# Performance work log

Measured on AMD Instinct MI355X. Metric: run time of the kernel, lower is better.

## Reference

```python
import jax, jax.numpy as jnp
import numpy as np

NX, NY = 512, 1024  # scaled grid (source used 128x256)
HID = 32


def _grid_edges(nx, ny):
    """Bidirectional 4-neighbor grid adjacency as [2, E] int32."""
    idx = np.arange(nx * ny).reshape(nx, ny)
    h_s, h_t = idx[:, :-1].ravel(), idx[:, 1:].ravel()
    v_s, v_t = idx[:-1, :].ravel(), idx[1:, :].ravel()
    src = np.concatenate([h_s, h_t, v_s, v_t])
    dst = np.concatenate([h_t, h_s, v_t, v_s])
    return jnp.asarray(np.stack([src, dst]), dtype=jnp.int32)


def setup_inputs() -> dict:
    key = jax.random.key(0)
    ks = jax.random.split(key, 8)

    def lin(k, fan_in, fan_out):
        bound = 1.0 / np.sqrt(fan_in)
        kw, kb = jax.random.split(k)
        w = jax.random.uniform(kw, (fan_in, fan_out), jnp.float32, -bound, bound)
        b = jax.random.uniform(kb, (fan_out,), jnp.float32, -bound, bound)
        return w, b

    inp = {}
    inp["x"] = jax.random.normal(ks[0], (NX * NY, 4), jnp.float32)
    inp["edge_index_0"] = _grid_edges(NX, NY)
    inp["edge_index_1"] = _grid_edges(NX // 2, NY // 2)
    inp["edge_index_2"] = _grid_edges(NX // 4, NY // 4)
    inp["fc1_w"], inp["fc1_b"] = lin(ks[1], 4, HID)
    for i in range(1, 6):
        inp[f"w{i}"], inp[f"b{i}"] = lin(ks[1 + i], HID, HID)
    inp["fc2_w"], inp["fc2_b"] = lin(ks[7], HID, 2)
    return inp


def gcn_conv(x, edge_index, w, b):
    """PyG GCNConv: self-loops + symmetric norm + linear + scatter-add + bias."""
    n = x.shape[0]
    loop = jnp.arange(n, dtype=edge_index.dtype)
    src = jnp.concatenate([edge_index[0], loop])
    dst = jnp.concatenate([edge_index[1], loop])
    deg = jax.ops.segment_sum(jnp.ones(dst.shape, x.dtype), dst, num_segments=n)
    dis = jax.lax.rsqrt(deg)  # deg >= 1 because of self-loops
    norm = dis[src] * dis[dst]  # [E+N]
    xw = x @ w  # [N, HID]
    out = jax.ops.segment_sum(xw[src] * norm[:, None], dst, num_segments=n)
    return out + b


def _upsample2(x):
    # Buffer-exact replica of torch `upsample(x, dim=2, channels=32, scale=2)`:
    # with `channels` doubling between iterations; then transpose + reshape.
    x = x.T  # [32, N]
    ch = HID
    for _ in range(2):
        x = jnp.repeat(x.reshape(ch, -1), 2, axis=-1)
        ch *= 2
    return x.T.reshape(-1, HID)  # [4N, 32]


def reference(x, edge_index_0, edge_index_1, edge_index_2,
              fc1_w, fc1_b, w1, b1, w2, b2, w3, b3, w4, b4, w5, b5,
              fc2_w, fc2_b):
    nx1, ny1 = NX // 2, NY // 2
    h = jax.nn.relu(x @ fc1_w + fc1_b)
    h = jax.nn.relu(gcn_conv(h, edge_index_0, w1, b1))            # level 0
    h1 = h.reshape(NX, NY, HID)[::2, ::2, :].reshape(-1, HID)     # down to level 1
    h1 = jax.nn.relu(gcn_conv(h1, edge_index_1, w2, b2))
    h2 = h1.reshape(nx1, ny1, HID)[::2, ::2, :].reshape(-1, HID)  # down to level 2
    h2 = jax.nn.relu(gcn_conv(h2, edge_index_2, w3, b3))
    h1u = h1 + _upsample2(h2)                                     # up to level 1
    h1u = jax.nn.relu(gcn_conv(h1u, edge_index_1, w4, b4))
    hu = h + _upsample2(h1u)                                      # up to level 0
    hu = jax.nn.relu(gcn_conv(hu, edge_index_0, w5, b5))
    return hu @ fc2_w + fc2_b  # [NX*NY, 2]
```

## Files before the change

### kernel.cpp

```cpp
#include <hip/hip_runtime.h>


#define TI 8
#define TJ 32

__device__ __forceinline__ float disf(int i, int j, int nx, int ny) {
  int deg = 1 + (i > 0) + (i < nx - 1) + (j > 0) + (j < ny - 1);
  return rsqrtf((float)deg);
}

__device__ __forceinline__ float4 f4z() { return make_float4(0.f, 0.f, 0.f, 0.f); }
__device__ __forceinline__ float4 f4fma(float s, float4 w, float4 a) {
  a.x = fmaf(s, w.x, a.x); a.y = fmaf(s, w.y, a.y);
  a.z = fmaf(s, w.z, a.z); a.w = fmaf(s, w.w, a.w);
  return a;
}
__device__ __forceinline__ float4 f4add(float4 a, float4 b) {
  return make_float4(a.x + b.x, a.y + b.y, a.z + b.z, a.w + b.w);
}
__device__ __forceinline__ float4 f4scale(float4 a, float s) {
  return make_float4(a.x * s, a.y * s, a.z * s, a.w * s);
}

template <int MODE, int NX, int NY, int NLOW>
__device__ __forceinline__ float4 load_u(
    const float* __restrict__ src, const float* __restrict__ low,
    const float4 (&f1c)[4], const float4& f1b, int gi, int gj, int c) {
  if (gi < 0 || gi >= NX || gj < 0 || gj >= NY) return f4z();
  const float d = disf(gi, gj, NX, NY);
  if constexpr (MODE == 0) {
    const float4 xv = ((const float4*)src)[gi * NY + gj];
    float4 h;
    h.x = fmaxf(fmaf(xv.x, f1c[0].x, fmaf(xv.y, f1c[1].x, fmaf(xv.z, f1c[2].x, fmaf(xv.w, f1c[3].x, f1b.x)))), 0.f);
    h.y = fmaxf(fmaf(xv.x, f1c[0].y, fmaf(xv.y, f1c[1].y, fmaf(xv.z, f1c[2].y, fmaf(xv.w, f1c[3].y, f1b.y)))), 0.f);
    h.z = fmaxf(fmaf(xv.x, f1c[0].z, fmaf(xv.y, f1c[1].z, fmaf(xv.z, f1c[2].z, fmaf(xv.w, f1c[3].z, f1b.z)))), 0.f);
    h.w = fmaxf(fmaf(xv.x, f1c[0].w, fmaf(xv.y, f1c[1].w, fmaf(xv.z, f1c[2].w, fmaf(xv.w, f1c[3].w, f1b.w)))), 0.f);
    return f4scale(h, d);
  } else if constexpr (MODE == 1) {
    const float4 v = ((const float4*)src)[((size_t)(2 * gi) * (2 * NY) + 2 * gj) * 8 + c];
    return f4scale(v, d);
  } else {
    const int r = gi * NY + gj;
    float4 v = ((const float4*)src)[(size_t)r * 8 + c];
    const int col = 16 * (r & 1) + 2 * c;
    const float2 E = *(const float2*)(low + (size_t)(r >> 3) * 32 + col);
    const float2 O = *(const float2*)(low + (size_t)((NLOW + (r >> 2)) >> 1) * 32 + col);
    v.x += E.x; v.y += O.x; v.z += E.y; v.w += O.y;
    return f4scale(v, d);
  }
}

template <int MODE, int NX, int NY, int NLOW>
__global__ __launch_bounds__(256, 4) void fused_gcn(
    const float* __restrict__ src, const float* __restrict__ low,
    const float* __restrict__ w, const float* __restrict__ bias,
    const float* __restrict__ fc1w, const float* __restrict__ fc1b,
    const float* __restrict__ fw2, const float* __restrict__ fb2,
    float* __restrict__ out) {
  __shared__ float sT[32][TI * TJ + 4];
  __shared__ float ldsW[1024];
  __shared__ float ldsB[104];

  const int t = threadIdx.x;
  ((float4*)ldsW)[t] = ((const float4*)w)[t];
  if (t < 32) ldsB[t] = bias[t];
  if constexpr (MODE == 3) {
    if (t >= 32 && t < 96) ldsB[t] = fw2[t - 32];
    if (t >= 96 && t < 98) ldsB[t] = fb2[t - 96];
  }

  const int jn = t >> 3, c = t & 7;
  const int j0 = blockIdx.x * TJ, i0 = blockIdx.y * TI;
  const int gj = j0 + jn;

  float4 f1c[4], f1b;
  if constexpr (MODE == 0) {
#pragma unroll
    for (int r = 0; r < 4; ++r) f1c[r] = *(const float4*)(fc1w + r * 32 + 4 * c);
    f1b = *(const float4*)(fc1b + 4 * c);
  }
  auto LOADU = [&](int a, int b) -> float4 {
    return load_u<MODE, NX, NY, NLOW>(src, low, f1c, f1b, a, b, c);
  };

  float4 up = LOADU(i0 - 1, gj);
  float4 uc = LOADU(i0, gj);
  float4 un = LOADU(i0 + 1, gj);
  float4 lf = LOADU(i0, gj - 1);
  float4 rt = LOADU(i0, gj + 1);

#pragma unroll
  for (int i = 0; i < TI; ++i) {
    const float4 sv = f4add(f4add(f4add(up, uc), f4add(un, lf)), rt);
    const int n = i * TJ + jn;
    sT[4 * c + 0][n] = sv.x; sT[4 * c + 1][n] = sv.y;
    sT[4 * c + 2][n] = sv.z; sT[4 * c + 3][n] = sv.w;
    if (i < TI - 1) {
      up = uc; uc = un;
      un = LOADU(i0 + i + 2, gj);
      lf = LOADU(i0 + i + 1, gj - 1);
      rt = LOADU(i0 + i + 1, gj + 1);
    }
  }
  __syncthreads();

  const int tn = t >> 2, tc = t & 3;
  float4 o00 = f4z(), o01 = f4z(), o10 = f4z(), o11 = f4z();
  float4 o20 = f4z(), o21 = f4z(), o30 = f4z(), o31 = f4z();
#pragma unroll
  for (int k = 0; k < 32; ++k) {
    const float4 sv = *(const float4*)&sT[k][4 * tn];
    const float4 w0 = *(const float4*)&ldsW[k * 32 + 8 * tc];
    const float4 w1 = *(const float4*)&ldsW[k * 32 + 8 * tc + 4];
    o00 = f4fma(sv.x, w0, o00); o01 = f4fma(sv.x, w1, o01);
    o10 = f4fma(sv.y, w0, o10); o11 = f4fma(sv.y, w1, o11);
    o20 = f4fma(sv.z, w0, o20); o21 = f4fma(sv.z, w1, o21);
    o30 = f4fma(sv.w, w0, o30); o31 = f4fma(sv.w, w1, o31);
  }
  const float4 b0 = *(const float4*)&ldsB[8 * tc];
  const float4 b1 = *(const float4*)&ldsB[8 * tc + 4];

  float4 fwA = f4z(), fwB = f4z(), fwC = f4z(), fwD = f4z();
  if constexpr (MODE == 3) {
    fwA = *(const float4*)&ldsB[32 + 16 * tc];
    fwB = *(const float4*)&ldsB[32 + 16 * tc + 4];
    fwC = *(const float4*)&ldsB[32 + 16 * tc + 8];
    fwD = *(const float4*)&ldsB[32 + 16 * tc + 12];
  }

  float4 oo[4][2] = {{o00, o01}, {o10, o11}, {o20, o21}, {o30, o31}};
  float a0[4], a1[4];
#pragma unroll
  for (int nn = 0; nn < 4; ++nn) {
    const int n = 4 * tn + nn;
    const int gi = i0 + (n >> 5), gjo = j0 + (n & 31);
    const float dv = disf(gi, gjo, NX, NY);
    float4 v0, v1;
    v0.x = fmaxf(fmaf(dv, oo[nn][0].x, b0.x), 0.f);
    v0.y = fmaxf(fmaf(dv, oo[nn][0].y, b0.y), 0.f);
    v0.z = fmaxf(fmaf(dv, oo[nn][0].z, b0.z), 0.f);
    v0.w = fmaxf(fmaf(dv, oo[nn][0].w, b0.w), 0.f);
    v1.x = fmaxf(fmaf(dv, oo[nn][1].x, b1.x), 0.f);
    v1.y = fmaxf(fmaf(dv, oo[nn][1].y, b1.y), 0.f);
    v1.z = fmaxf(fmaf(dv, oo[nn][1].z, b1.z), 0.f);
    v1.w = fmaxf(fmaf(dv, oo[nn][1].w, b1.w), 0.f);
    if constexpr (MODE != 3) {
      float* op = out + (size_t)(gi * NY + gjo) * 32 + 8 * tc;
      *(float4*)op = v0;
      *(float4*)(op + 4) = v1;
    } else {
      a0[nn] = v0.x * fwA.x + v0.y * fwA.z + v0.z * fwB.x + v0.w * fwB.z +
               v1.x * fwC.x + v1.y * fwC.z + v1.z * fwD.x + v1.w * fwD.z;
      a1[nn] = v0.x * fwA.y + v0.y * fwA.w + v0.z * fwB.y + v0.w * fwB.w +
               v1.x * fwC.y + v1.y * fwC.w + v1.z * fwD.y + v1.w * fwD.w;
    }
  }
  if constexpr (MODE == 3) {
#pragma unroll
    for (int nn = 0; nn < 4; ++nn) {
      a0[nn] += __shfl_xor(a0[nn], 1, 64); a0[nn] += __shfl_xor(a0[nn], 2, 64);
      a1[nn] += __shfl_xor(a1[nn], 1, 64); a1[nn] += __shfl_xor(a1[nn], 2, 64);
    }
    if (tc == 0) {
      const float fb0 = ldsB[96], fb1 = ldsB[97];
#pragma unroll
      for (int nn = 0; nn < 4; ++nn) {
        const int n = 4 * tn + nn;
        const int gi = i0 + (n >> 5), gjo = j0 + (n & 31);
        ((float2*)out)[gi * NY + gjo] = make_float2(a0[nn] + fb0, a1[nn] + fb1);
      }
    }
  }
}

#define N0 (512 * 1024)
#define N1 (256 * 512)
#define N2 (128 * 256)

extern "C" void kernel_launch(void* const* d_in, const int* in_sizes, int n_in,
                              void* d_out, int out_size, void* d_ws, size_t ws_size,
                              hipStream_t stream) {
  const float* x    = (const float*)d_in[0];
  const float* fc1w = (const float*)d_in[4];
  const float* fc1b = (const float*)d_in[5];
  const float* w1 = (const float*)d_in[6];
  const float* b1 = (const float*)d_in[7];
  const float* w2 = (const float*)d_in[8];
  const float* b2 = (const float*)d_in[9];
  const float* w3 = (const float*)d_in[10];
  const float* b3 = (const float*)d_in[11];
  const float* w4 = (const float*)d_in[12];
  const float* b4 = (const float*)d_in[13];
  const float* w5 = (const float*)d_in[14];
  const float* b5 = (const float*)d_in[15];
  const float* fw2 = (const float*)d_in[16];
  const float* fb2 = (const float*)d_in[17];

  float* ws = (float*)d_ws;
  const size_t S0 = (size_t)N0 * 32, S1 = (size_t)N1 * 32, S2 = (size_t)N2 * 32;
  float* h   = ws;
  float* h1  = ws + S0;
  float* h2  = ws + S0 + S1;
  float* h1u = ws + S0 + S1 + S2;
  float* outp = (float*)d_out;

  fused_gcn<0, 512, 1024, 0><<<dim3(1024 / TJ, 512 / TI), 256, 0, stream>>>(
      x, nullptr, w1, b1, fc1w, fc1b, nullptr, nullptr, h);
  fused_gcn<1, 256, 512, 0><<<dim3(512 / TJ, 256 / TI), 256, 0, stream>>>(
      h, nullptr, w2, b2, nullptr, nullptr, nullptr, nullptr, h1);
  fused_gcn<1, 128, 256, 0><<<dim3(256 / TJ, 128 / TI), 256, 0, stream>>>(
      h1, nullptr, w3, b3, nullptr, nullptr, nullptr, nullptr, h2);
  fused_gcn<2, 256, 512, N2><<<dim3(512 / TJ, 256 / TI), 256, 0, stream>>>(
      h1, h2, w4, b4, nullptr, nullptr, nullptr, nullptr, h1u);
  fused_gcn<3, 512, 1024, N1><<<dim3(1024 / TJ, 512 / TI), 256, 0, stream>>>(
      h, h1u, w5, b5, nullptr, nullptr, fw2, fb2, outp);
}
```

Measured before the change: 218.8 us.

## Halve row tile, remap block IDs for XCD locality, two nodes per thread

Shrinks the tile to 4 rows so each thread computes two nodes instead of four in the 32x32 transform, cutting accumulator registers, and raises the launch-bounds occupancy hint to 6 blocks. Block IDs are swizzled so consecutive tiles are spread in strided groups of eight, aiming to keep spatial neighbours on the same XCD/L2 for halo reuse. LDS padding changes to one float and the final output stores are packed into wider vectors. Smaller tiles add proportionally more halo reloads and per-block weight staging.

```diff
diff --git a/kernel.cpp b/kernel.cpp
--- a/kernel.cpp
+++ b/kernel.cpp
@@ -1,7 +1,7 @@
 #include <hip/hip_runtime.h>
 
 
-#define TI 8
+#define TI 4
 #define TJ 32
 
 __device__ __forceinline__ float disf(int i, int j, int nx, int ny) {
@@ -51,13 +51,13 @@
 }
 
 template <int MODE, int NX, int NY, int NLOW>
-__global__ __launch_bounds__(256, 4) void fused_gcn(
+__global__ __launch_bounds__(256, 6) void fused_gcn(
     const float* __restrict__ src, const float* __restrict__ low,
     const float* __restrict__ w, const float* __restrict__ bias,
     const float* __restrict__ fc1w, const float* __restrict__ fc1b,
     const float* __restrict__ fw2, const float* __restrict__ fb2,
     float* __restrict__ out) {
-  __shared__ float sT[32][TI * TJ + 4];
+  __shared__ float sT[32][TI * TJ + 1];
   __shared__ float ldsW[1024];
   __shared__ float ldsB[104];
 
@@ -69,8 +69,16 @@
     if (t >= 96 && t < 98) ldsB[t] = fb2[t - 96];
   }
 
+  constexpr int GX = NY / TJ;
+  constexpr int GY = NX / TI;
+  constexpr int NWG = GX * GY;
+  constexpr int LGX = (GX == 8) ? 3 : ((GX == 16) ? 4 : 5);
+  const int bid = blockIdx.y * GX + blockIdx.x;
+  const int sw = (bid & 7) * (NWG >> 3) + (bid >> 3);
+  const int j0 = (sw & (GX - 1)) * TJ;
+  const int i0 = (sw >> LGX) * TI;
+
   const int jn = t >> 3, c = t & 7;
-  const int j0 = blockIdx.x * TJ, i0 = blockIdx.y * TI;
   const int gj = j0 + jn;
 
   float4 f1c[4], f1b;
@@ -104,71 +112,63 @@
   }
   __syncthreads();
 
-  const int tn = t >> 2, tc = t & 3;
-  float4 o00 = f4z(), o01 = f4z(), o10 = f4z(), o11 = f4z();
-  float4 o20 = f4z(), o21 = f4z(), o30 = f4z(), o31 = f4z();
+  const int p = t >> 2, tc = t & 3;
+  float4 oA0 = f4z(), oA1 = f4z(), oB0 = f4z(), oB1 = f4z();
 #pragma unroll
   for (int k = 0; k < 32; ++k) {
-    const float4 sv = *(const float4*)&sT[k][4 * tn];
+    const float sa = sT[k][2 * p];
+    const float sb = sT[k][2 * p + 1];
     const float4 w0 = *(const float4*)&ldsW[k * 32 + 8 * tc];
     const float4 w1 = *(const float4*)&ldsW[k * 32 + 8 * tc + 4];
-    o00 = f4fma(sv.x, w0, o00); o01 = f4fma(sv.x, w1, o01);
-    o10 = f4fma(sv.y, w0, o10); o11 = f4fma(sv.y, w1, o11);
-    o20 = f4fma(sv.z, w0, o20); o21 = f4fma(sv.z, w1, o21);
-    o30 = f4fma(sv.w, w0, o30); o31 = f4fma(sv.w, w1, o31);
+    oA0 = f4fma(sa, w0, oA0); oA1 = f4fma(sa, w1, oA1);
+    oB0 = f4fma(sb, w0, oB0); oB1 = f4fma(sb, w1, oB1);
   }
   const float4 b0 = *(const float4*)&ldsB[8 * tc];
   const float4 b1 = *(const float4*)&ldsB[8 * tc + 4];
 
-  float4 fwA = f4z(), fwB = f4z(), fwC = f4z(), fwD = f4z();
-  if constexpr (MODE == 3) {
-    fwA = *(const float4*)&ldsB[32 + 16 * tc];
-    fwB = *(const float4*)&ldsB[32 + 16 * tc + 4];
-    fwC = *(const float4*)&ldsB[32 + 16 * tc + 8];
-    fwD = *(const float4*)&ldsB[32 + 16 * tc + 12];
-  }
-
-  float4 oo[4][2] = {{o00, o01}, {o10, o11}, {o20, o21}, {o30, o31}};
-  float a0[4], a1[4];
-#pragma unroll
-  for (int nn = 0; nn < 4; ++nn) {
-    const int n = 4 * tn + nn;
-    const int gi = i0 + (n >> 5), gjo = j0 + (n & 31);
-    const float dv = disf(gi, gjo, NX, NY);
-    float4 v0, v1;
-    v0.x = fmaxf(fmaf(dv, oo[nn][0].x, b0.x), 0.f);
-    v0.y = fmaxf(fmaf(dv, oo[nn][0].y, b0.y), 0.f);
-    v0.z = fmaxf(fmaf(dv, oo[nn][0].z, b0.z), 0.f);
-    v0.w = fmaxf(fmaf(dv, oo[nn][0].w, b0.w), 0.f);
-    v1.x = fmaxf(fmaf(dv, oo[nn][1].x, b1.x), 0.f);
-    v1.y = fmaxf(fmaf(dv, oo[nn][1].y, b1.y), 0.f);
-    v1.z = fmaxf(fmaf(dv, oo[nn][1].z, b1.z), 0.f);
-    v1.w = fmaxf(fmaf(dv, oo[nn][1].w, b1.w), 0.f);
-    if constexpr (MODE != 3) {
-      float* op = out + (size_t)(gi * NY + gjo) * 32 + 8 * tc;
-      *(float4*)op = v0;
-      *(float4*)(op + 4) = v1;
-    } else {
-      a0[nn] = v0.x * fwA.x + v0.y * fwA.z + v0.z * fwB.x + v0.w * fwB.z +
-               v1.x * fwC.x + v1.y * fwC.z + v1.z * fwD.x + v1.w * fwD.z;
-      a1[nn] = v0.x * fwA.y + v0.y * fwA.w + v0.z * fwB.y + v0.w * fwB.w +
-               v1.x * fwC.y + v1.y * fwC.w + v1.z * fwD.y + v1.w * fwD.w;
-    }
-  }
-  if constexpr (MODE == 3) {
-#pragma unroll
-    for (int nn = 0; nn < 4; ++nn) {
-      a0[nn] += __shfl_xor(a0[nn], 1, 64); a0[nn] += __shfl_xor(a0[nn], 2, 64);
-      a1[nn] += __shfl_xor(a1[nn], 1, 64); a1[nn] += __shfl_xor(a1[nn], 2, 64);
-    }
+  const int nA = 2 * p;
+  const int gi = i0 + (nA >> 5);
+  const int gjA = j0 + (nA & 31);
+  const float dA = disf(gi, gjA, NX, NY);
+  const float dB = disf(gi, gjA + 1, NX, NY);
+
+  float4 vA0, vA1, vB0, vB1;
+  vA0.x = fmaxf(fmaf(dA, oA0.x, b0.x), 0.f); vA0.y = fmaxf(fmaf(dA, oA0.y, b0.y), 0.f);
+  vA0.z = fmaxf(fmaf(dA, oA0.z, b0.z), 0.f); vA0.w = fmaxf(fmaf(dA, oA0.w, b0.w), 0.f);
+  vA1.x = fmaxf(fmaf(dA, oA1.x, b1.x), 0.f); vA1.y = fmaxf(fmaf(dA, oA1.y, b1.y), 0.f);
+  vA1.z = fmaxf(fmaf(dA, oA1.z, b1.z), 0.f); vA1.w = fmaxf(fmaf(dA, oA1.w, b1.w), 0.f);
+  vB0.x = fmaxf(fmaf(dB, oB0.x, b0.x), 0.f); vB0.y = fmaxf(fmaf(dB, oB0.y, b0.y), 0.f);
+  vB0.z = fmaxf(fmaf(dB, oB0.z, b0.z), 0.f); vB0.w = fmaxf(fmaf(dB, oB0.w, b0.w), 0.f);
+  vB1.x = fmaxf(fmaf(dB, oB1.x, b1.x), 0.f); vB1.y = fmaxf(fmaf(dB, oB1.y, b1.y), 0.f);
+  vB1.z = fmaxf(fmaf(dB, oB1.z, b1.z), 0.f); vB1.w = fmaxf(fmaf(dB, oB1.w, b1.w), 0.f);
+
+  if constexpr (MODE != 3) {
+    float* opA = out + (size_t)(gi * NY + gjA) * 32 + 8 * tc;
+    *(float4*)opA = vA0;
+    *(float4*)(opA + 4) = vA1;
+    *(float4*)(opA + 32) = vB0;
+    *(float4*)(opA + 36) = vB1;
+  } else {
+    const float4 fwA = *(const float4*)&ldsB[32 + 16 * tc];
+    const float4 fwB = *(const float4*)&ldsB[32 + 16 * tc + 4];
+    const float4 fwC = *(const float4*)&ldsB[32 + 16 * tc + 8];
+    const float4 fwD = *(const float4*)&ldsB[32 + 16 * tc + 12];
+    float a0A = vA0.x * fwA.x + vA0.y * fwA.z + vA0.z * fwB.x + vA0.w * fwB.z +
+                vA1.x * fwC.x + vA1.y * fwC.z + vA1.z * fwD.x + vA1.w * fwD.z;
+    float a1A = vA0.x * fwA.y + vA0.y * fwA.w + vA0.z * fwB.y + vA0.w * fwB.w +
+                vA1.x * fwC.y + vA1.y * fwC.w + vA1.z * fwD.y + vA1.w * fwD.w;
+    float a0B = vB0.x * fwA.x + vB0.y * fwA.z + vB0.z * fwB.x + vB0.w * fwB.z +
+                vB1.x * fwC.x + vB1.y * fwC.z + vB1.z * fwD.x + vB1.w * fwD.z;
+    float a1B = vB0.x * fwA.y + vB0.y * fwA.w + vB0.z * fwB.y + vB0.w * fwB.w +
+                vB1.x * fwC.y + vB1.y * fwC.w + vB1.z * fwD.y + vB1.w * fwD.w;
+    a0A += __shfl_xor(a0A, 1, 64); a0A += __shfl_xor(a0A, 2, 64);
+    a1A += __shfl_xor(a1A, 1, 64); a1A += __shfl_xor(a1A, 2, 64);
+    a0B += __shfl_xor(a0B, 1, 64); a0B += __shfl_xor(a0B, 2, 64);
+    a1B += __shfl_xor(a1B, 1, 64); a1B += __shfl_xor(a1B, 2, 64);
     if (tc == 0) {
       const float fb0 = ldsB[96], fb1 = ldsB[97];
-#pragma unroll
-      for (int nn = 0; nn < 4; ++nn) {
-        const int n = 4 * tn + nn;
-        const int gi = i0 + (n >> 5), gjo = j0 + (n & 31);
-        ((float2*)out)[gi * NY + gjo] = make_float2(a0[nn] + fb0, a1[nn] + fb1);
-      }
+      const float4 r = make_float4(a0A + fb0, a1A + fb1, a0B + fb0, a1B + fb1);
+      ((float4*)out)[(gi * NY + gjA) >> 1] = r;
     }
   }
 }
```

Result: faster. 208.5 us (-4.7%).
